# Kernel optimization log

Measured on AMD Instinct MI355X. Metric: run time of the kernel, lower is better.

## Reference

```python
import jax, jax.numpy as jnp
import numpy as np

N_HEAD = 16
N_KV_HEAD = 4
HEAD_DIM = 128
EPS = 1e-6


def apply_rotary_emb(x, cos, sin):
    # x: (B,T,H,hd); cos/sin: (1,T,1,hd//2)
    d = x.shape[3] // 2
    x1, x2 = x[..., :d], x[..., d:]
    y1 = x1 * cos + x2 * sin
    y2 = x1 * -sin + x2 * cos
    return jnp.concatenate([y1, y2], axis=3).astype(x.dtype)


def rmsnorm(x):
    # flax nnx.RMSNorm with use_scale=False: x * rsqrt(mean(x^2) + eps)
    ms = jnp.mean(jnp.square(x), axis=-1, keepdims=True)
    return (x * jax.lax.rsqrt(ms + EPS)).astype(x.dtype)


def setup_inputs() -> dict:
    key = jax.random.key(0)
    ks = jax.random.split(key, 7)
    B, T, C = 4, 2048, 2048
    s = 0.02
    return {
        "x": jax.random.normal(ks[0], (B, T, C), jnp.float32),
        "cos": jax.random.normal(ks[1], (1, T, 1, HEAD_DIM // 2), jnp.float32),
        "sin": jax.random.normal(ks[2], (1, T, 1, HEAD_DIM // 2), jnp.float32),
        "Wq": jax.random.normal(ks[3], (C, N_HEAD * HEAD_DIM), jnp.float32) * s,
        "Wk": jax.random.normal(ks[4], (C, N_KV_HEAD * HEAD_DIM), jnp.float32) * s,
        "Wv": jax.random.normal(ks[5], (C, N_KV_HEAD * HEAD_DIM), jnp.float32) * s,
        "Wo": jax.random.normal(ks[6], (C, C), jnp.float32) * s,
    }


def reference(x, cos, sin, Wq, Wk, Wv, Wo):
    B, T, C = x.shape
    q = (x @ Wq).reshape(B, T, N_HEAD, HEAD_DIM)
    k = (x @ Wk).reshape(B, T, N_KV_HEAD, HEAD_DIM)
    v = (x @ Wv).reshape(B, T, N_KV_HEAD, HEAD_DIM)
    q = rmsnorm(apply_rotary_emb(q, cos, sin))
    k = rmsnorm(apply_rotary_emb(k, cos, sin))
    # (B,H,T,hd)
    q = jnp.transpose(q, (0, 2, 1, 3))
    k = jnp.transpose(k, (0, 2, 1, 3))
    v = jnp.transpose(v, (0, 2, 1, 3))
    nrep = N_HEAD // N_KV_HEAD
    k = jnp.repeat(k, nrep, axis=1)
    v = jnp.repeat(v, nrep, axis=1)
    scale = 1.0 / jnp.sqrt(jnp.float32(HEAD_DIM))
    att = jnp.einsum('bhqd,bhkd->bhqk', q, k) * scale
    mask = jnp.tril(jnp.ones((T, T), dtype=bool))[None, None, :, :]
    att = jnp.where(mask, att, -jnp.inf)
    att = jax.nn.softmax(att, axis=-1)
    y = jnp.einsum('bhqk,bhkd->bhqd', att, v)
    y = jnp.transpose(y, (0, 2, 1, 3)).reshape(B, T, -1)
    return y @ Wo
```

## Files before the change

kernel.cpp:

```cpp
#include <hip/hip_runtime.h>
#include <hip/hip_bf16.h>

typedef __attribute__((ext_vector_type(8))) short short8;
typedef __attribute__((ext_vector_type(4))) float f32x4;
typedef __attribute__((ext_vector_type(16))) float f32x16;

#define B_SZ 4
#define T_SEQ 2048
#define C_DIM 2048
#define NH 16
#define NKV 4
#define HD 128

#define MFMA16 __builtin_amdgcn_mfma_f32_16x16x32_bf16
#define MFMA32 __builtin_amdgcn_mfma_f32_32x32x16_bf16

__device__ __forceinline__ unsigned short f2bf(float f) {
  union { __hip_bfloat16 h; unsigned short u; } v;
  v.h = __float2bfloat16(f);
  return v.u;
}
__device__ __forceinline__ float bf2f(unsigned short u) {
  union { unsigned short u; __hip_bfloat16 h; } v;
  v.u = u;
  return __bfloat162float(v.h);
}
__device__ __forceinline__ unsigned pkbf(float lo, float hi) {
  return (unsigned)f2bf(lo) | ((unsigned)f2bf(hi) << 16);
}

__device__ __forceinline__ void gload_lds16(const unsigned short* g, unsigned short* l) {
  __builtin_amdgcn_global_load_lds(
      (const __attribute__((address_space(1))) unsigned int*)g,
      (__attribute__((address_space(3))) unsigned int*)l, 16, 0, 0);
}

__global__ void cast_x(const float* __restrict__ x, unsigned short* __restrict__ xb, int n4) {
  int i = blockIdx.x * blockDim.x + threadIdx.x;
  if (i < n4) {
    float4 f = ((const float4*)x)[i];
    ushort4 u = make_ushort4(f2bf(f.x), f2bf(f.y), f2bf(f.z), f2bf(f.w));
    ((ushort4*)xb)[i] = u;
  }
}

__global__ void wtransAll(const float* __restrict__ Wq, const float* __restrict__ Wk,
                          const float* __restrict__ Wv, const float* __restrict__ Wo,
                          unsigned short* __restrict__ WqkvT, unsigned short* __restrict__ WoT) {
  __shared__ float tile[32][33];
  int y = blockIdx.y;
  const float* W;
  unsigned short* Wt;
  int N, n0;
  if (y < 64) { W = Wq; Wt = WqkvT; N = 2048; n0 = y * 32; }
  else if (y < 80) { W = Wk; Wt = WqkvT + (size_t)2048 * 2048; N = 512; n0 = (y - 64) * 32; }
  else if (y < 96) { W = Wv; Wt = WqkvT + (size_t)2560 * 2048; N = 512; n0 = (y - 80) * 32; }
  else { W = Wo; Wt = WoT; N = 2048; n0 = (y - 96) * 32; }
  int k0 = blockIdx.x * 32;
  int tx = threadIdx.x, ty = threadIdx.y;
#pragma unroll
  for (int i = 0; i < 4; i++)
    tile[ty + i * 8][tx] = W[(size_t)(k0 + ty + i * 8) * N + n0 + tx];
  __syncthreads();
#pragma unroll
  for (int i = 0; i < 4; i++)
    Wt[(size_t)(n0 + ty + i * 8) * 2048 + k0 + tx] = f2bf(tile[tx][ty + i * 8]);
}

__global__ void vtrans(const unsigned short* __restrict__ qkv, unsigned short* __restrict__ Vt) {
  __shared__ unsigned short tile[32][34];
  int t0 = blockIdx.x * 32, d0 = blockIdx.y * 32;
  int b = blockIdx.z >> 2, kvh = blockIdx.z & 3;
  int tx = threadIdx.x, ty = threadIdx.y;
#pragma unroll
  for (int i = 0; i < 4; i++)
    tile[ty + i * 8][tx] =
        qkv[(size_t)(b * T_SEQ + t0 + ty + i * 8) * 3072 + 2560 + kvh * HD + d0 + tx];
  __syncthreads();
#pragma unroll
  for (int i = 0; i < 4; i++)
    Vt[((size_t)(b * NKV + kvh) * HD + d0 + ty + i * 8) * T_SEQ + t0 + tx] = tile[tx][ty + i * 8];
}

template <typename OutT>
__global__ __launch_bounds__(512, 2) void gemm128(const unsigned short* __restrict__ A,
                                                  const unsigned short* __restrict__ Bt,
                                                  OutT* __restrict__ Cc, int N, int K, int GX) {
  __shared__ alignas(16) unsigned short lds[2][3][128 * 64];
  const int tid = threadIdx.x, lane = tid & 63, wid = tid >> 6;
  const int wave_m = wid >> 2, wave_n = wid & 3;
  const int r16 = lane & 15, q4 = lane >> 4;
  const int sw = r16 & 7;

  int nwg = gridDim.x, orig = blockIdx.x;
  int qq = nwg >> 3, rr = nwg & 7;
  int xcd = orig & 7, loc = orig >> 3;
  int wg = (xcd < rr ? xcd * (qq + 1) : rr * (qq + 1) + (xcd - rr) * qq) + loc;
  int bx = wg % GX, by = wg / GX;
  const size_t row0 = (size_t)bx * 128, col0 = (size_t)by * 256;

  const unsigned short* Ab = A + row0 * K;
  const unsigned short* Bb0 = Bt + col0 * K;
  const unsigned short* Bb1 = Bt + (col0 + 128) * K;

  const int srow = lane >> 3, spb = lane & 7;
  auto stage = [&](const unsigned short* base, int buf, int slot, int k0) {
#pragma unroll
    for (int j = 0; j < 2; ++j) {
      int cw = j * 8 + wid;
      int row = cw * 8 + srow;
      gload_lds16(base + (size_t)row * K + k0 + ((spb ^ srow) * 8), &lds[buf][slot][cw * 512]);
    }
  };

  f32x4 acc[4][4];
  f32x4 zero = {0.f, 0.f, 0.f, 0.f};
#pragma unroll
  for (int m = 0; m < 4; m++)
#pragma unroll
    for (int n = 0; n < 4; n++) acc[m][n] = zero;

  const int NT = K / 64;
  stage(Ab, 0, 0, 0);
  stage(Bb0, 0, 1, 0);
  stage(Bb1, 0, 2, 0);
  stage(Ab, 1, 0, 64);
  asm volatile("s_waitcnt vmcnt(2)" ::: "memory");
  __builtin_amdgcn_s_barrier();

  short8 af[4][2], b01[2][2], b23[2][2];
  const int bslot = 1 + (wave_n >> 1);
  const int bro = (wave_n & 1) * 64;

  int cur = 0;
#pragma unroll 1
  for (int t = 0; t < NT; ++t) {
    const unsigned short* Ah = &lds[cur][0][0];
    const unsigned short* Bh = &lds[cur][bslot][0];
    const int k1 = t * 64 + 64, k2 = t * 64 + 128;
#pragma unroll
    for (int mf = 0; mf < 4; mf++)
#pragma unroll
      for (int kk = 0; kk < 2; kk++)
        af[mf][kk] =
            *(const short8*)(Ah + (wave_m * 64 + mf * 16 + r16) * 64 + (((kk * 4 + q4) ^ sw) * 8));
#pragma unroll
    for (int nf = 0; nf < 2; nf++)
#pragma unroll
      for (int kk = 0; kk < 2; kk++)
        b01[nf][kk] =
            *(const short8*)(Bh + (bro + nf * 16 + r16) * 64 + (((kk * 4 + q4) ^ sw) * 8));
    if (t + 1 < NT) stage(Bb0, cur ^ 1, 1, k1);
    __builtin_amdgcn_s_barrier();
    asm volatile("s_waitcnt lgkmcnt(0)" ::: "memory");
    __builtin_amdgcn_s_setprio(1);
#pragma unroll
    for (int mf = 0; mf < 4; mf++)
#pragma unroll
      for (int nf = 0; nf < 2; nf++)
#pragma unroll
        for (int kk = 0; kk < 2; kk++)
          acc[mf][nf] = MFMA16(af[mf][kk], b01[nf][kk], acc[mf][nf], 0, 0, 0);
    __builtin_amdgcn_s_setprio(0);
    __builtin_amdgcn_s_barrier();
#pragma unroll
    for (int nf = 0; nf < 2; nf++)
#pragma unroll
      for (int kk = 0; kk < 2; kk++)
        b23[nf][kk] =
            *(const short8*)(Bh + (bro + (nf + 2) * 16 + r16) * 64 + (((kk * 4 + q4) ^ sw) * 8));
    if (t + 1 < NT) stage(Bb1, cur ^ 1, 2, k1);
    if (t + 2 < NT) stage(Ab, cur, 0, k2);
    __builtin_amdgcn_s_barrier();
    asm volatile("s_waitcnt lgkmcnt(0)" ::: "memory");
    __builtin_amdgcn_s_setprio(1);
#pragma unroll
    for (int mf = 0; mf < 4; mf++)
#pragma unroll
      for (int nf = 0; nf < 2; nf++)
#pragma unroll
        for (int kk = 0; kk < 2; kk++)
          acc[mf][nf + 2] = MFMA16(af[mf][kk], b23[nf][kk], acc[mf][nf + 2], 0, 0, 0);
    __builtin_amdgcn_s_setprio(0);
    if (t + 2 < NT)
      asm volatile("s_waitcnt vmcnt(2)" ::: "memory");
    else if (t + 1 < NT)
      asm volatile("s_waitcnt vmcnt(0)" ::: "memory");
    __builtin_amdgcn_s_barrier();
    cur ^= 1;
  }

#pragma unroll
  for (int mf = 0; mf < 4; mf++)
#pragma unroll
    for (int nf = 0; nf < 4; nf++) {
      size_t rbase = row0 + wave_m * 64 + mf * 16 + q4 * 4;
      size_t cc = col0 + wave_n * 64 + nf * 16 + r16;
#pragma unroll
      for (int jj = 0; jj < 4; jj++) {
        if constexpr (sizeof(OutT) == 2)
          Cc[(rbase + jj) * (size_t)N + cc] = f2bf(acc[mf][nf][jj]);
        else
          Cc[(rbase + jj) * (size_t)N + cc] = acc[mf][nf][jj];
      }
    }
}

template <typename OutT>
__global__ __launch_bounds__(512, 2) void gemm256(const unsigned short* __restrict__ A,
                                                  const unsigned short* __restrict__ Bt,
                                                  OutT* __restrict__ Cc, int N, int K, int GX) {
  __shared__ alignas(16) unsigned short lds[2][4][128 * 64];
  const int tid = threadIdx.x, lane = tid & 63, wid = tid >> 6;
  const int wave_m = wid >> 2, wave_n = wid & 3;
  const int r16 = lane & 15, q4 = lane >> 4;
  const int sw = r16 & 7;

  int nwg = gridDim.x, orig = blockIdx.x;
  int qq = nwg >> 3, rr = nwg & 7;
  int xcd = orig & 7, loc = orig >> 3;
  int wg = (xcd < rr ? xcd * (qq + 1) : rr * (qq + 1) + (xcd - rr) * qq) + loc;
  int bx = wg % GX, by = wg / GX;
  const size_t row0 = (size_t)bx * 256, col0 = (size_t)by * 256;

  const unsigned short* Ab0 = A + row0 * K;
  const unsigned short* Ab1 = A + (row0 + 128) * K;
  const unsigned short* Bb0 = Bt + col0 * K;
  const unsigned short* Bb1 = Bt + (col0 + 128) * K;

  const int srow = lane >> 3, spb = lane & 7;
  auto stage = [&](const unsigned short* base, int buf, int slot, int k0) {
#pragma unroll
    for (int j = 0; j < 2; ++j) {
      int cw = j * 8 + wid;
      int row = cw * 8 + srow;
      gload_lds16(base + (size_t)row * K + k0 + ((spb ^ srow) * 8), &lds[buf][slot][cw * 512]);
    }
  };

  f32x4 acc[8][4];
  f32x4 zero = {0.f, 0.f, 0.f, 0.f};
#pragma unroll
  for (int m = 0; m < 8; m++)
#pragma unroll
    for (int n = 0; n < 4; n++) acc[m][n] = zero;

  const int NT = K / 64;
  stage(Ab0, 0, 0, 0);
  stage(Ab1, 0, 1, 0);
  stage(Bb0, 0, 2, 0);
  stage(Bb1, 0, 3, 0);
  stage(Ab0, 1, 0, 64);
  stage(Ab1, 1, 1, 64);
  asm volatile("s_waitcnt vmcnt(4)" ::: "memory");
  __builtin_amdgcn_s_barrier();

  short8 af[4][2], b01[2][2], b23[2][2];
  const int bslot = 2 + (wave_n >> 1);
  const int bro = (wave_n & 1) * 64;

  int cur = 0;
#pragma unroll 1
  for (int t = 0; t < NT; ++t) {
    const unsigned short* Ah = &lds[cur][wave_m][0];
    const unsigned short* Bh = &lds[cur][bslot][0];
    const int k1 = t * 64 + 64, k2 = t * 64 + 128;
#pragma unroll
    for (int mf = 0; mf < 4; mf++)
#pragma unroll
      for (int kk = 0; kk < 2; kk++)
        af[mf][kk] = *(const short8*)(Ah + (mf * 16 + r16) * 64 + (((kk * 4 + q4) ^ sw) * 8));
#pragma unroll
    for (int nf = 0; nf < 2; nf++)
#pragma unroll
      for (int kk = 0; kk < 2; kk++)
        b01[nf][kk] =
            *(const short8*)(Bh + (bro + nf * 16 + r16) * 64 + (((kk * 4 + q4) ^ sw) * 8));
    if (t + 1 < NT) stage(Bb0, cur ^ 1, 2, k1);
    __builtin_amdgcn_s_barrier();
    asm volatile("s_waitcnt lgkmcnt(0)" ::: "memory");
    __builtin_amdgcn_s_setprio(1);
#pragma unroll
    for (int mf = 0; mf < 4; mf++)
#pragma unroll
      for (int nf = 0; nf < 2; nf++)
#pragma unroll
        for (int kk = 0; kk < 2; kk++)
          acc[mf][nf] = MFMA16(af[mf][kk], b01[nf][kk], acc[mf][nf], 0, 0, 0);
    __builtin_amdgcn_s_setprio(0);
    __builtin_amdgcn_s_barrier();
#pragma unroll
    for (int nf = 0; nf < 2; nf++)
#pragma unroll
      for (int kk = 0; kk < 2; kk++)
        b23[nf][kk] =
            *(const short8*)(Bh + (bro + (nf + 2) * 16 + r16) * 64 + (((kk * 4 + q4) ^ sw) * 8));
    if (t + 1 < NT) stage(Bb1, cur ^ 1, 3, k1);
    __builtin_amdgcn_s_barrier();
    asm volatile("s_waitcnt lgkmcnt(0)" ::: "memory");
    __builtin_amdgcn_s_setprio(1);
#pragma unroll
    for (int mf = 0; mf < 4; mf++)
#pragma unroll
      for (int nf = 0; nf < 2; nf++)
#pragma unroll
        for (int kk = 0; kk < 2; kk++)
          acc[mf][nf + 2] = MFMA16(af[mf][kk], b23[nf][kk], acc[mf][nf + 2], 0, 0, 0);
    __builtin_amdgcn_s_setprio(0);
    __builtin_amdgcn_s_barrier();
#pragma unroll
    for (int mf = 0; mf < 4; mf++)
#pragma unroll
      for (int kk = 0; kk < 2; kk++)
        af[mf][kk] =
            *(const short8*)(Ah + ((mf + 4) * 16 + r16) * 64 + (((kk * 4 + q4) ^ sw) * 8));
    __builtin_amdgcn_s_barrier();
    asm volatile("s_waitcnt lgkmcnt(0)" ::: "memory");
    __builtin_amdgcn_s_setprio(1);
#pragma unroll
    for (int mf = 0; mf < 4; mf++)
#pragma unroll
      for (int nf = 0; nf < 2; nf++)
#pragma unroll
        for (int kk = 0; kk < 2; kk++)
          acc[mf + 4][nf] = MFMA16(af[mf][kk], b01[nf][kk], acc[mf + 4][nf], 0, 0, 0);
    __builtin_amdgcn_s_setprio(0);
    __builtin_amdgcn_s_barrier();
    if (t + 2 < NT) {
      stage(Ab0, cur, 0, k2);
      stage(Ab1, cur, 1, k2);
    }
    __builtin_amdgcn_s_barrier();
    __builtin_amdgcn_s_setprio(1);
#pragma unroll
    for (int mf = 0; mf < 4; mf++)
#pragma unroll
      for (int nf = 0; nf < 2; nf++)
#pragma unroll
        for (int kk = 0; kk < 2; kk++)
          acc[mf + 4][nf + 2] = MFMA16(af[mf][kk], b23[nf][kk], acc[mf + 4][nf + 2], 0, 0, 0);
    __builtin_amdgcn_s_setprio(0);
    if (t + 1 < NT) {
      if (t + 2 < NT)
        asm volatile("s_waitcnt vmcnt(4)" ::: "memory");
      else
        asm volatile("s_waitcnt vmcnt(0)" ::: "memory");
    }
    __builtin_amdgcn_s_barrier();
    cur ^= 1;
  }

#pragma unroll
  for (int mf = 0; mf < 8; mf++)
#pragma unroll
    for (int nf = 0; nf < 4; nf++) {
      size_t rbase = row0 + wave_m * 128 + mf * 16 + q4 * 4;
      size_t cc = col0 + wave_n * 64 + nf * 16 + r16;
#pragma unroll
      for (int jj = 0; jj < 4; jj++) {
        if constexpr (sizeof(OutT) == 2)
          Cc[(rbase + jj) * (size_t)N + cc] = f2bf(acc[mf][nf][jj]);
        else
          Cc[(rbase + jj) * (size_t)N + cc] = acc[mf][nf][jj];
      }
    }
}

__global__ void ropeAll(const unsigned short* __restrict__ qkv, const float* __restrict__ cosp,
                        const float* __restrict__ sinp, unsigned short* __restrict__ Qb,
                        unsigned short* __restrict__ Kb) {
  int gid = blockIdx.x * 4 + (threadIdx.x >> 6);
  int lane = threadIdx.x & 63;
  int hh = gid % 20;
  int bt = gid / 20;
  int t = bt % T_SEQ, b = bt / T_SEQ;
  int colbase;
  unsigned short* dst;
  float outscale;
  if (hh < 16) {
    colbase = hh * HD;
    dst = Qb + ((size_t)(b * NH + hh) * T_SEQ + t) * HD;
    outscale = 0.08838834764831845f;
  } else {
    int h2 = hh - 16;
    colbase = 2048 + h2 * HD;
    dst = Kb + ((size_t)(b * NKV + h2) * T_SEQ + t) * HD;
    outscale = 1.0f;
  }
  const unsigned short* src = qkv + (size_t)(b * T_SEQ + t) * 3072 + colbase;
  float x1 = bf2f(src[lane]), x2 = bf2f(src[64 + lane]);
  float c = cosp[t * 64 + lane], s = sinp[t * 64 + lane];
  float y1 = x1 * c + x2 * s;
  float y2 = x2 * c - x1 * s;
  float ss = y1 * y1 + y2 * y2;
#pragma unroll
  for (int d = 1; d < 64; d <<= 1) ss += __shfl_xor(ss, d);
  float r = rsqrtf(ss * (1.f / 128.f) + 1e-6f) * outscale;
  dst[lane] = f2bf(y1 * r);
  dst[64 + lane] = f2bf(y2 * r);
}

__global__ __launch_bounds__(256, 2) void attn(const unsigned short* __restrict__ Qn,
                                               const unsigned short* __restrict__ Kn,
                                               const unsigned short* __restrict__ Vt,
                                               unsigned short* __restrict__ Y) {
  __shared__ alignas(16) unsigned short lK[2][64 * 128];
  __shared__ alignas(16) unsigned short lV[2][128 * 64];

  int lin = blockIdx.x;
  int low3 = lin & 7, rest = lin >> 3;
  int chi = rest >> 6, idx = rest & 63;
  int c = (chi << 3) | low3;
  int b = c >> 2, kvh = c & 3;
  int h = kvh * 4 + (idx >> 4);
  int qt = 15 - (idx & 15);
  int Q0 = qt * 128;

  int lane = threadIdx.x & 63, w = threadIdx.x >> 6;
  const int q5 = lane & 31, hi = lane >> 5, l7 = lane & 7;
  const int qrow = Q0 + w * 32 + q5;
  const unsigned short* Qp = Qn + ((size_t)(b * NH + h) * T_SEQ + qrow) * HD;
  const unsigned short* Kp = Kn + (size_t)(b * NKV + kvh) * T_SEQ * HD;
  const unsigned short* Vp = Vt + (size_t)(b * NKV + kvh) * HD * T_SEQ;

  short8 qf[8];
#pragma unroll
  for (int i = 0; i < 8; i++) qf[i] = *(const short8*)(Qp + i * 16 + hi * 8);

  f32x16 o4[4];
#pragma unroll
  for (int d = 0; d < 4; d++)
#pragma unroll
    for (int r = 0; r < 16; r++) o4[d][r] = 0.f;
  float mrow = -1e30f, Lp = 0.f;

  auto stageK = [&](int kv0, int buf) {
#pragma unroll
    for (int j = 0; j < 4; ++j) {
      int cw = w * 4 + j;
      int row = cw * 4 + (lane >> 4);
      int cb = lane & 15;
      gload_lds16(Kp + (size_t)(kv0 + row) * HD + ((cb ^ (row & 7)) * 8), &lK[buf][cw * 512]);
    }
  };
  auto stageV = [&](int kv0, int buf) {
#pragma unroll
    for (int j = 0; j < 4; ++j) {
      int cw = w * 4 + j;
      int row = cw * 8 + (lane >> 3);
      int db = lane & 7;
      gload_lds16(Vp + (size_t)row * T_SEQ + kv0 + ((db ^ (row & 7)) * 8), &lV[buf][cw * 512]);
    }
  };

  const int ntiles = 2 * qt + 2;
  const int ntw = (Q0 + w * 32 + 95) >> 6;

  stageK(0, 0);
  stageV(0, 0);
  __syncthreads();
  int cur = 0;

  for (int t = 0; t < ntiles; ++t) {
    int kv0 = t * 64;
    if (t + 1 < ntiles) { stageK(kv0 + 64, cur ^ 1); stageV(kv0 + 64, cur ^ 1); }
    if (t < ntw) {
#pragma unroll
      for (int kt = 0; kt < 2; kt++) {
        f32x16 st;
#pragma unroll
        for (int r = 0; r < 16; r++) st[r] = 0.f;
        const int krow = kt * 32 + q5;
        __builtin_amdgcn_s_setprio(1);
#pragma unroll
        for (int i = 0; i < 8; i++) {
          short8 kf = *(const short8*)(&lK[cur][krow * 128 + (((2 * i + hi) ^ l7) * 8)]);
          st = MFMA32(kf, qf[i], st, 0, 0, 0);
        }
        __builtin_amdgcn_s_setprio(0);
        if (kv0 + kt * 32 + 31 > Q0 + w * 32) {
#pragma unroll
          for (int r = 0; r < 16; r++) {
            int kg = kv0 + kt * 32 + (r & 3) + 8 * (r >> 2) + 4 * hi;
            if (kg > qrow) st[r] = -1e30f;
          }
        }
        float pm = st[0];
#pragma unroll
        for (int r = 1; r < 16; r++) pm = fmaxf(pm, st[r]);
        pm = fmaxf(pm, __shfl_xor(pm, 32));
        if (!__all(pm - mrow <= 8.0f)) {
          float mn = fmaxf(mrow, pm);
          float al = __expf(mrow - mn);
          mrow = mn;
          Lp *= al;
#pragma unroll
          for (int d = 0; d < 4; d++)
#pragma unroll
            for (int r = 0; r < 16; r++) o4[d][r] *= al;
        }
        float p[16];
#pragma unroll
        for (int r = 0; r < 16; r++) {
          p[r] = __expf(st[r] - mrow);
          Lp += p[r];
        }
#pragma unroll
        for (int ks = 0; ks < 2; ks++) {
          unsigned x0 = pkbf(p[8 * ks + 0], p[8 * ks + 1]);
          unsigned x1 = pkbf(p[8 * ks + 2], p[8 * ks + 3]);
          unsigned y0 = pkbf(p[8 * ks + 4], p[8 * ks + 5]);
          unsigned y1 = pkbf(p[8 * ks + 6], p[8 * ks + 7]);
          unsigned sx0 = __shfl_xor((int)x0, 32), sx1 = __shfl_xor((int)x1, 32);
          unsigned sy0 = __shfl_xor((int)y0, 32), sy1 = __shfl_xor((int)y1, 32);
          union { unsigned u[4]; short8 s; } pw;
          pw.u[0] = hi ? sy0 : x0;
          pw.u[1] = hi ? sy1 : x1;
          pw.u[2] = hi ? y0 : sx0;
          pw.u[3] = hi ? y1 : sx1;
          const int cb = 4 * kt + 2 * ks + hi;
          __builtin_amdgcn_s_setprio(1);
#pragma unroll
          for (int db = 0; db < 4; db++) {
            int vrow = db * 32 + q5;
            short8 vf = *(const short8*)(&lV[cur][vrow * 64 + ((cb ^ l7) * 8)]);
            o4[db] = MFMA32(vf, pw.s, o4[db], 0, 0, 0);
          }
          __builtin_amdgcn_s_setprio(0);
        }
      }
    }
    __syncthreads();
    cur ^= 1;
  }

  float L = Lp + __shfl_xor(Lp, 32);
  float linv = 1.f / L;
  unsigned short* Yp = Y + ((size_t)(b * T_SEQ) + qrow) * (NH * HD) + h * HD;
#pragma unroll
  for (int db = 0; db < 4; db++)
#pragma unroll
    for (int g = 0; g < 4; g++) {
      int d0 = db * 32 + g * 8 + 4 * hi;
      ushort4 v = make_ushort4(f2bf(o4[db][g * 4 + 0] * linv), f2bf(o4[db][g * 4 + 1] * linv),
                               f2bf(o4[db][g * 4 + 2] * linv), f2bf(o4[db][g * 4 + 3] * linv));
      *(ushort4*)(Yp + d0) = v;
    }
}

extern "C" void kernel_launch(void* const* d_in, const int* in_sizes, int n_in,
                              void* d_out, int out_size, void* d_ws, size_t ws_size,
                              hipStream_t stream) {
  const float* x = (const float*)d_in[0];
  const float* cosp = (const float*)d_in[1];
  const float* sinp = (const float*)d_in[2];
  const float* Wq = (const float*)d_in[3];
  const float* Wk = (const float*)d_in[4];
  const float* Wv = (const float*)d_in[5];
  const float* Wo = (const float*)d_in[6];
  float* out = (float*)d_out;

  char* ws = (char*)d_ws;
  size_t off = 0;
  auto alloc = [&](size_t bytes) { void* p = ws + off; off += bytes; return p; };
  const size_t BT = (size_t)B_SZ * T_SEQ;
  unsigned short* xb = (unsigned short*)alloc(BT * C_DIM * 2);
  unsigned short* WqkvT = (unsigned short*)alloc((size_t)3072 * 2048 * 2);
  unsigned short* WoT = (unsigned short*)alloc((size_t)2048 * 2048 * 2);
  unsigned short* qkv = (unsigned short*)alloc(BT * 3072 * 2);
  unsigned short* Kb = (unsigned short*)alloc(BT * 512 * 2);
  unsigned short* Vb = (unsigned short*)alloc(BT * 512 * 2);
  unsigned short* Qb = xb;
  unsigned short* Yb = qkv;

  dim3 tb(32, 8);
  cast_x<<<16384, 256, 0, stream>>>(x, xb, (int)(BT * C_DIM / 4));
  wtransAll<<<dim3(64, 160), tb, 0, stream>>>(Wq, Wk, Wv, Wo, WqkvT, WoT);

  gemm128<unsigned short><<<768, 512, 0, stream>>>(xb, WqkvT, qkv, 3072, 2048, 64);

  ropeAll<<<(B_SZ * T_SEQ * 20) / 4, 256, 0, stream>>>(qkv, cosp, sinp, Qb, Kb);
  vtrans<<<dim3(64, 4, 16), tb, 0, stream>>>(qkv, Vb);

  attn<<<dim3(1024), 256, 0, stream>>>(Qb, Kb, Vb, Yb);

  gemm256<float><<<256, 512, 0, stream>>>(Yb, WoT, out, 2048, 2048, 32);
}
```

Before: 395.9 us.

## Merge cast and weight-transpose kernels; shrink attention KV tile to 32

The x cast and the weight transposes now run as one launch, with blocks split by index, which removes one kernel launch. The attention kernel now stages 32-key K/V tiles instead of 64, using a new 4-way XOR swizzle for V. Each block uses half the LDS and the causal work is split more finely. In exchange there are twice as many barrier iterations and the per-tile staging loads are smaller.

```diff
diff --git a/kernel.cpp b/kernel.cpp
--- a/kernel.cpp
+++ b/kernel.cpp
@@ -35,20 +35,21 @@
       (__attribute__((address_space(3))) unsigned int*)l, 16, 0, 0);
 }
 
-__global__ void cast_x(const float* __restrict__ x, unsigned short* __restrict__ xb, int n4) {
-  int i = blockIdx.x * blockDim.x + threadIdx.x;
-  if (i < n4) {
+__global__ void prep(const float* __restrict__ x, unsigned short* __restrict__ xb,
+                     const float* __restrict__ Wq, const float* __restrict__ Wk,
+                     const float* __restrict__ Wv, const float* __restrict__ Wo,
+                     unsigned short* __restrict__ WqkvT, unsigned short* __restrict__ WoT) {
+  int bid = blockIdx.x, tid = threadIdx.x;
+  if (bid < 16384) {
+    int i = bid * 256 + tid;
     float4 f = ((const float4*)x)[i];
     ushort4 u = make_ushort4(f2bf(f.x), f2bf(f.y), f2bf(f.z), f2bf(f.w));
     ((ushort4*)xb)[i] = u;
+    return;
   }
-}
-
-__global__ void wtransAll(const float* __restrict__ Wq, const float* __restrict__ Wk,
-                          const float* __restrict__ Wv, const float* __restrict__ Wo,
-                          unsigned short* __restrict__ WqkvT, unsigned short* __restrict__ WoT) {
   __shared__ float tile[32][33];
-  int y = blockIdx.y;
+  int idx = bid - 16384;
+  int y = idx >> 6, kx = idx & 63;
   const float* W;
   unsigned short* Wt;
   int N, n0;
@@ -56,8 +57,8 @@
   else if (y < 80) { W = Wk; Wt = WqkvT + (size_t)2048 * 2048; N = 512; n0 = (y - 64) * 32; }
   else if (y < 96) { W = Wv; Wt = WqkvT + (size_t)2560 * 2048; N = 512; n0 = (y - 80) * 32; }
   else { W = Wo; Wt = WoT; N = 2048; n0 = (y - 96) * 32; }
-  int k0 = blockIdx.x * 32;
-  int tx = threadIdx.x, ty = threadIdx.y;
+  int k0 = kx * 32;
+  int tx = tid & 31, ty = tid >> 5;
 #pragma unroll
   for (int i = 0; i < 4; i++)
     tile[ty + i * 8][tx] = W[(size_t)(k0 + ty + i * 8) * N + n0 + tx];
@@ -404,8 +405,8 @@
                                                const unsigned short* __restrict__ Kn,
                                                const unsigned short* __restrict__ Vt,
                                                unsigned short* __restrict__ Y) {
-  __shared__ alignas(16) unsigned short lK[2][64 * 128];
-  __shared__ alignas(16) unsigned short lV[2][128 * 64];
+  __shared__ alignas(16) unsigned short lK[2][32 * 128];
+  __shared__ alignas(16) unsigned short lV[2][128 * 32];
 
   int lin = blockIdx.x;
   int low3 = lin & 7, rest = lin >> 3;
@@ -436,8 +437,8 @@
 
   auto stageK = [&](int kv0, int buf) {
 #pragma unroll
-    for (int j = 0; j < 4; ++j) {
-      int cw = w * 4 + j;
+    for (int j = 0; j < 2; ++j) {
+      int cw = w * 2 + j;
       int row = cw * 4 + (lane >> 4);
       int cb = lane & 15;
       gload_lds16(Kp + (size_t)(kv0 + row) * HD + ((cb ^ (row & 7)) * 8), &lK[buf][cw * 512]);
@@ -445,16 +446,16 @@
   };
   auto stageV = [&](int kv0, int buf) {
 #pragma unroll
-    for (int j = 0; j < 4; ++j) {
-      int cw = w * 4 + j;
-      int row = cw * 8 + (lane >> 3);
-      int db = lane & 7;
-      gload_lds16(Vp + (size_t)row * T_SEQ + kv0 + ((db ^ (row & 7)) * 8), &lV[buf][cw * 512]);
+    for (int j = 0; j < 2; ++j) {
+      int cw = w * 2 + j;
+      int row = cw * 16 + (lane >> 2);
+      int ts = lane & 3;
+      gload_lds16(Vp + (size_t)row * T_SEQ + kv0 + ((ts ^ (row & 3)) * 8), &lV[buf][cw * 512]);
     }
   };
 
-  const int ntiles = 2 * qt + 2;
-  const int ntw = (Q0 + w * 32 + 95) >> 6;
+  const int ntiles = 4 * qt + 4;
+  const int ntw = (Q0 + w * 32 + 63) >> 5;
 
   stageK(0, 0);
   stageV(0, 0);
@@ -462,72 +463,68 @@
   int cur = 0;
 
   for (int t = 0; t < ntiles; ++t) {
-    int kv0 = t * 64;
-    if (t + 1 < ntiles) { stageK(kv0 + 64, cur ^ 1); stageV(kv0 + 64, cur ^ 1); }
+    int kv0 = t * 32;
+    if (t + 1 < ntiles) { stageK(kv0 + 32, cur ^ 1); stageV(kv0 + 32, cur ^ 1); }
     if (t < ntw) {
-#pragma unroll
-      for (int kt = 0; kt < 2; kt++) {
-        f32x16 st;
-#pragma unroll
-        for (int r = 0; r < 16; r++) st[r] = 0.f;
-        const int krow = kt * 32 + q5;
+      f32x16 st;
+#pragma unroll
+      for (int r = 0; r < 16; r++) st[r] = 0.f;
+      __builtin_amdgcn_s_setprio(1);
+#pragma unroll
+      for (int i = 0; i < 8; i++) {
+        short8 kf = *(const short8*)(&lK[cur][q5 * 128 + (((2 * i + hi) ^ l7) * 8)]);
+        st = MFMA32(kf, qf[i], st, 0, 0, 0);
+      }
+      __builtin_amdgcn_s_setprio(0);
+      if (kv0 + 31 > Q0 + w * 32) {
+#pragma unroll
+        for (int r = 0; r < 16; r++) {
+          int kg = kv0 + (r & 3) + 8 * (r >> 2) + 4 * hi;
+          if (kg > qrow) st[r] = -1e30f;
+        }
+      }
+      float pm = st[0];
+#pragma unroll
+      for (int r = 1; r < 16; r++) pm = fmaxf(pm, st[r]);
+      pm = fmaxf(pm, __shfl_xor(pm, 32));
+      if (!__all(pm - mrow <= 8.0f)) {
+        float mn = fmaxf(mrow, pm);
+        float al = __expf(mrow - mn);
+        mrow = mn;
+        Lp *= al;
+#pragma unroll
+        for (int d = 0; d < 4; d++)
+#pragma unroll
+          for (int r = 0; r < 16; r++) o4[d][r] *= al;
+      }
+      float p[16];
+#pragma unroll
+      for (int r = 0; r < 16; r++) {
+        p[r] = __expf(st[r] - mrow);
+        Lp += p[r];
+      }
+#pragma unroll
+      for (int ks = 0; ks < 2; ks++) {
+        unsigned x0 = pkbf(p[8 * ks + 0], p[8 * ks + 1]);
+        unsigned x1 = pkbf(p[8 * ks + 2], p[8 * ks + 3]);
+        unsigned y0 = pkbf(p[8 * ks + 4], p[8 * ks + 5]);
+        unsigned y1 = pkbf(p[8 * ks + 6], p[8 * ks + 7]);
+        unsigned sx0 = __shfl_xor((int)x0, 32), sx1 = __shfl_xor((int)x1, 32);
+        unsigned sy0 = __shfl_xor((int)y0, 32), sy1 = __shfl_xor((int)y1, 32);
+        union { unsigned u[4]; short8 s; } pw;
+        pw.u[0] = hi ? sy0 : x0;
+        pw.u[1] = hi ? sy1 : x1;
+        pw.u[2] = hi ? y0 : sx0;
+        pw.u[3] = hi ? y1 : sx1;
+        const int cb = 2 * ks + hi;
         __builtin_amdgcn_s_setprio(1);
 #pragma unroll
-        for (int i = 0; i < 8; i++) {
-          short8 kf = *(const short8*)(&lK[cur][krow * 128 + (((2 * i + hi) ^ l7) * 8)]);
-          st = MFMA32(kf, qf[i], st, 0, 0, 0);
+        for (int db = 0; db < 4; db++) {
+          int vrow = db * 32 + q5;
+          short8 vf = *(const short8*)(&lV[cur][vrow * 32 + ((cb ^ (vrow & 3)) * 8)]);
+          o4[db] = MFMA32(vf, pw.s, o4[db], 0, 0, 0);
         }
         __builtin_amdgcn_s_setprio(0);
-        if (kv0 + kt * 32 + 31 > Q0 + w * 32) {
-#pragma unroll
-          for (int r = 0; r < 16; r++) {
-            int kg = kv0 + kt * 32 + (r & 3) + 8 * (r >> 2) + 4 * hi;
-            if (kg > qrow) st[r] = -1e30f;
-          }
-        }
-        float pm = st[0];
-#pragma unroll
-        for (int r = 1; r < 16; r++) pm = fmaxf(pm, st[r]);
-        pm = fmaxf(pm, __shfl_xor(pm, 32));
-        if (!__all(pm - mrow <= 8.0f)) {
-          float mn = fmaxf(mrow, pm);
-          float al = __expf(mrow - mn);
-          mrow = mn;
-          Lp *= al;
-#pragma unroll
-          for (int d = 0; d < 4; d++)
-#pragma unroll
-            for (int r = 0; r < 16; r++) o4[d][r] *= al;
-        }
-        float p[16];
-#pragma unroll
-        for (int r = 0; r < 16; r++) {
-          p[r] = __expf(st[r] - mrow);
-          Lp += p[r];
-        }
-#pragma unroll
-        for (int ks = 0; ks < 2; ks++) {
-          unsigned x0 = pkbf(p[8 * ks + 0], p[8 * ks + 1]);
-          unsigned x1 = pkbf(p[8 * ks + 2], p[8 * ks + 3]);
-          unsigned y0 = pkbf(p[8 * ks + 4], p[8 * ks + 5]);
-          unsigned y1 = pkbf(p[8 * ks + 6], p[8 * ks + 7]);
-          unsigned sx0 = __shfl_xor((int)x0, 32), sx1 = __shfl_xor((int)x1, 32);
-          unsigned sy0 = __shfl_xor((int)y0, 32), sy1 = __shfl_xor((int)y1, 32);
-          union { unsigned u[4]; short8 s; } pw;
-          pw.u[0] = hi ? sy0 : x0;
-          pw.u[1] = hi ? sy1 : x1;
-          pw.u[2] = hi ? y0 : sx0;
-          pw.u[3] = hi ? y1 : sx1;
-          const int cb = 4 * kt + 2 * ks + hi;
-          __builtin_amdgcn_s_setprio(1);
-#pragma unroll
-          for (int db = 0; db < 4; db++) {
-            int vrow = db * 32 + q5;
-            short8 vf = *(const short8*)(&lV[cur][vrow * 64 + ((cb ^ l7) * 8)]);
-            o4[db] = MFMA32(vf, pw.s, o4[db], 0, 0, 0);
-          }
-          __builtin_amdgcn_s_setprio(0);
-        }
       }
     }
     __syncthreads();
@@ -574,8 +571,7 @@
   unsigned short* Yb = qkv;
 
   dim3 tb(32, 8);
-  cast_x<<<16384, 256, 0, stream>>>(x, xb, (int)(BT * C_DIM / 4));
-  wtransAll<<<dim3(64, 160), tb, 0, stream>>>(Wq, Wk, Wv, Wo, WqkvT, WoT);
+  prep<<<26624, 256, 0, stream>>>(x, xb, Wq, Wk, Wv, Wo, WqkvT, WoT);
 
   gemm128<unsigned short><<<768, 512, 0, stream>>>(xb, WqkvT, qkv, 3072, 2048, 64);
 
```

After: 393.2 us. About the same (-0.7%).
